# Kernel optimization log

Hardware: AMD Instinct MI355X
Metric: run time of the kernel (lower is better)

Reference implementation:

```python
import jax, jax.numpy as jnp
import numpy as np

N_NODES = 100000
N_EDGES = 1600000
HID = 256
HEADS = 4
HEAD_DIM = HID // HEADS
EPS = 1e-5


def _layernorm(x, g, b):
    mu = jnp.mean(x, axis=-1, keepdims=True)
    var = jnp.mean(jnp.square(x - mu), axis=-1, keepdims=True)
    return (x - mu) * jax.lax.rsqrt(var + EPS) * g + b


def setup_inputs() -> dict:
    key = jax.random.key(0)
    ks = jax.random.split(key, 16)
    s = 0.05  # small init, mimics xavier gain=0.1
    inp = {
        'h': jax.random.normal(ks[0], (N_NODES, HID), jnp.float32),
        'src': jax.random.randint(ks[1], (N_EDGES,), 0, N_NODES, jnp.int32),
        'dst': jax.random.randint(ks[2], (N_EDGES,), 0, N_NODES, jnp.int32),
        'Wq': jax.random.normal(ks[3], (HID, HID), jnp.float32) * s,
        'bq': jnp.zeros((HID,), jnp.float32),
        'Wk': jax.random.normal(ks[4], (HID, HID), jnp.float32) * s,
        'bk': jnp.zeros((HID,), jnp.float32),
        'Wv': jax.random.normal(ks[5], (HID, HID), jnp.float32) * s,
        'bv': jnp.zeros((HID,), jnp.float32),
        'Wo': jax.random.normal(ks[6], (HID, HID), jnp.float32) * s,
        'bo': jnp.zeros((HID,), jnp.float32),
        'W1': jax.random.normal(ks[7], (HID, 2 * HID), jnp.float32) * s,
        'b1': jnp.zeros((2 * HID,), jnp.float32),
        'W2': jax.random.normal(ks[8], (2 * HID, HID), jnp.float32) * s,
        'b2': jnp.zeros((HID,), jnp.float32),
        'g1': jnp.ones((HID,), jnp.float32),
        'be1': jnp.zeros((HID,), jnp.float32),
        'g2': jnp.ones((HID,), jnp.float32),
        'be2': jnp.zeros((HID,), jnp.float32),
    }
    return inp


def reference(h, src, dst, Wq, bq, Wk, bk, Wv, bv, Wo, bo, W1, b1, W2, b2, g1, be1, g2, be2):
    N = h.shape[0]
    scale = HEAD_DIM ** -0.5
    h_norm = _layernorm(h, g1, be1)
    Q = (h_norm @ Wq + bq).reshape(N, HEADS, HEAD_DIM)
    K = (h_norm @ Wk + bk).reshape(N, HEADS, HEAD_DIM)
    V = (h_norm @ Wv + bv).reshape(N, HEADS, HEAD_DIM)

    # per-edge attention logits: q from dst, k from src  -> [E, heads]
    logits = jnp.einsum('ehd,ehd->eh', Q[dst], K[src]) * scale

    # edge softmax grouped by destination node (dgl.ops.edge_softmax)
    seg_max = jax.ops.segment_max(logits, dst, num_segments=N)  # [N, heads]
    e = jnp.exp(logits - seg_max[dst])
    seg_sum = jax.ops.segment_sum(e, dst, num_segments=N)
    w = e / seg_sum[dst]  # [E, heads]

    # message = V[src] * attn ; aggregate by sum over incoming edges
    msg = V[src] * w[:, :, None]  # [E, heads, head_dim]
    h_new = jax.ops.segment_sum(msg, dst, num_segments=N).reshape(N, HID)

    h_attn = h_new @ Wo + bo
    h = h + h_attn  # dropout is identity in eval
    h2 = _layernorm(h, g2, be2)
    ffn = jax.nn.relu(h2 @ W1 + b1) @ W2 + b2
    return h + ffn
```

## Files before the change

### kernel.cpp

```cpp
#include <hip/hip_runtime.h>
#include <hip/hip_bf16.h>

#define NN 100000
#define NE 1600000

typedef __attribute__((ext_vector_type(8))) short bf16x8;
typedef __attribute__((ext_vector_type(4))) float f32x4;
typedef __attribute__((ext_vector_type(2))) float f32x2;
typedef __attribute__((ext_vector_type(2))) unsigned int u32x2;
typedef __attribute__((ext_vector_type(4))) unsigned int u32x4;

__device__ __forceinline__ float bf2f(unsigned short u) {
    union { unsigned int i; float f; } c; c.i = ((unsigned int)u) << 16; return c.f;
}
__device__ __forceinline__ unsigned short f2bf(float f) {
    union { float f; unsigned int i; } c; c.f = f;
    unsigned int lsb = (c.i >> 16) & 1u;
    c.i += 0x7FFFu + lsb;
    return (unsigned short)(c.i >> 16);
}
__device__ __forceinline__ u32x4 pack8bf(f32x4 a, f32x4 b) {
    u32x4 p;
    p.x = f2bf(a[0]) | ((unsigned int)f2bf(a[1]) << 16);
    p.y = f2bf(a[2]) | ((unsigned int)f2bf(a[3]) << 16);
    p.z = f2bf(b[0]) | ((unsigned int)f2bf(b[1]) << 16);
    p.w = f2bf(b[2]) | ((unsigned int)f2bf(b[3]) << 16);
    return p;
}
__device__ __forceinline__ void gload_lds16(const void* g, void* l) {
    __builtin_amdgcn_global_load_lds(
        (const __attribute__((address_space(1))) void*)g,
        (__attribute__((address_space(3))) void*)l, 16, 0, 0);
}

__global__ __launch_bounds__(256) void ln_k(
    const float* __restrict__ x, const float* __restrict__ g,
    const float* __restrict__ b, unsigned short* __restrict__ y, int nrows)
{
    int w = threadIdx.x >> 6, lane = threadIdx.x & 63;
    int row = blockIdx.x * 4 + w;
    if (row >= nrows) return;
    const float4 xv = *(const float4*)(x + (size_t)row * 256 + lane * 4);
    float s  = xv.x + xv.y + xv.z + xv.w;
    float sq = xv.x*xv.x + xv.y*xv.y + xv.z*xv.z + xv.w*xv.w;
    #pragma unroll
    for (int m = 1; m < 64; m <<= 1) {
        s  += __shfl_xor(s,  m);
        sq += __shfl_xor(sq, m);
    }
    float mu  = s * (1.0f / 256.0f);
    float var = sq * (1.0f / 256.0f) - mu * mu;
    float r = rsqrtf(var + 1e-5f);
    float4 gv = *(const float4*)(g + lane * 4);
    float4 bv = *(const float4*)(b + lane * 4);
    ushort4 o;
    o.x = f2bf((xv.x - mu) * r * gv.x + bv.x);
    o.y = f2bf((xv.y - mu) * r * gv.y + bv.y);
    o.z = f2bf((xv.z - mu) * r * gv.z + bv.z);
    o.w = f2bf((xv.w - mu) * r * gv.w + bv.w);
    *(ushort4*)(y + (size_t)row * 256 + lane * 4) = o;
}

__global__ __launch_bounds__(256) void wcv_all_k(
    const float* __restrict__ Wq, const float* __restrict__ Wk, const float* __restrict__ Wv,
    const float* __restrict__ Wo, const float* __restrict__ W1, const float* __restrict__ W2,
    unsigned short* __restrict__ Wqkvt, unsigned short* __restrict__ Wot,
    unsigned short* __restrict__ W1t, unsigned short* __restrict__ W2t,
    const float* __restrict__ bq, const float* __restrict__ bk, const float* __restrict__ bv,
    float* __restrict__ bqkv)
{
    int id = blockIdx.x;
    int t = threadIdx.x;
    if (id == 512) {
        bqkv[t] = bq[t]; bqkv[256 + t] = bk[t]; bqkv[512 + t] = bv[t];
        return;
    }
    const float* W; unsigned short* Wt; int K, N, kx, ny;
    if (id < 192) {
        int grp = id >> 6, l = id & 63;
        W = (grp == 0) ? Wq : ((grp == 1) ? Wk : Wv);
        Wt = Wqkvt + grp * 256 * 256;
        K = 256; N = 256; kx = l & 7; ny = l >> 3;
    } else if (id < 256) {
        int l = id - 192; W = Wo; Wt = Wot; K = 256; N = 256; kx = l & 7; ny = l >> 3;
    } else if (id < 384) {
        int l = id - 256; W = W1; Wt = W1t; K = 256; N = 512; kx = l & 7; ny = l >> 3;
    } else {
        int l = id - 384; W = W2; Wt = W2t; K = 512; N = 256; kx = l & 15; ny = l >> 4;
    }
    __shared__ unsigned short tl[32][33];
    int bk2 = kx * 32, bn = ny * 32;
    int lx = t & 31, ly = t >> 5;
    #pragma unroll
    for (int r = 0; r < 32; r += 8)
        tl[ly + r][lx] = f2bf(W[(size_t)(bk2 + ly + r) * N + bn + lx]);
    __syncthreads();
    #pragma unroll
    for (int r = 0; r < 32; r += 8)
        Wt[(size_t)(bn + ly + r) * K + bk2 + lx] = tl[lx][ly + r];
}

template<int OMODE, bool RELU, bool RES>
__global__ __launch_bounds__(512) void mgemm_k(
    const unsigned short* __restrict__ A, const unsigned short* __restrict__ Wt,
    const float* __restrict__ bias, void* __restrict__ outv, void* __restrict__ out2,
    const void* __restrict__ res, const float* __restrict__ g, const float* __restrict__ be,
    int M, int N, int K)
{
    __shared__ __align__(16) char lds[49152];
    const int t = threadIdx.x;
    const int lane = t & 63;
    const int wid = t >> 6;
    const int wm = wid >> 2, wn = wid & 3;
    const int bm = blockIdx.y * 128, bn = blockIdx.x * 256;

    f32x4 acc[4][4] = {};

    const int ra_s = t >> 2;
    const int sa_s = (t & 3) ^ (ra_s & 3);
    const size_t arow = (size_t)min(bm + ra_s, M - 1) * K + sa_s * 8;
    const int rb0 = t >> 2;
    const int sb0 = (t & 3) ^ (rb0 & 3);
    const int rb1 = (512 + t) >> 2;
    const int sb1 = (t & 3) ^ (rb1 & 3);
    const size_t brow0 = (size_t)(bn + rb0) * K + sb0 * 8;
    const size_t brow1 = (size_t)(bn + rb1) * K + sb1 * 8;

    const int fr = lane & 15, fs = lane >> 4;
    const int rslot = fs ^ (fr & 3);

    const int KS = K >> 5;
    int cur = 0;
    {
        unsigned short* Ab = (unsigned short*)(lds);
        unsigned short* Bb = (unsigned short*)(lds + 16384);
        gload_lds16(A + arow, Ab + t * 8);
        gload_lds16(Wt + brow0, Bb + t * 8);
        gload_lds16(Wt + brow1, Bb + (512 + t) * 8);
    }
    for (int ks = 0; ks < KS; ++ks) {
        __syncthreads();
        if (ks + 1 < KS) {
            int k1 = (ks + 1) << 5;
            unsigned short* Ab = (unsigned short*)(lds + (cur ^ 1) * 8192);
            unsigned short* Bb = (unsigned short*)(lds + 16384 + (cur ^ 1) * 16384);
            gload_lds16(A + arow + k1, Ab + t * 8);
            gload_lds16(Wt + brow0 + k1, Bb + t * 8);
            gload_lds16(Wt + brow1 + k1, Bb + (512 + t) * 8);
        }
        const unsigned short* As = (const unsigned short*)(lds + cur * 8192);
        const unsigned short* Bs = (const unsigned short*)(lds + 16384 + cur * 16384);
        bf16x8 af[4], bf[4];
        #pragma unroll
        for (int fm = 0; fm < 4; ++fm)
            af[fm] = *(const bf16x8*)&As[(wm * 64 + fm * 16 + fr) * 32 + rslot * 8];
        #pragma unroll
        for (int fn = 0; fn < 4; ++fn)
            bf[fn] = *(const bf16x8*)&Bs[(wn * 64 + fn * 16 + fr) * 32 + rslot * 8];
        #pragma unroll
        for (int fm = 0; fm < 4; ++fm)
            #pragma unroll
            for (int fn = 0; fn < 4; ++fn)
                acc[fm][fn] = __builtin_amdgcn_mfma_f32_16x16x32_bf16(
                    af[fm], bf[fn], acc[fm][fn], 0, 0, 0);
        cur ^= 1;
    }
    __syncthreads();

    float* wl = (float*)(lds + wid * 4352);
    float* stats = (float*)(lds + 34816);
    const int rr = lane >> 2;
    const int c4 = (lane & 3) * 16;
    const int qg = lane >> 4;

    #pragma unroll
    for (int fm = 0; fm < 4; ++fm) {
        #pragma unroll
        for (int fn = 0; fn < 4; ++fn)
            #pragma unroll
            for (int i = 0; i < 4; ++i)
                wl[(qg * 4 + i) * 68 + fn * 16 + fr] = acc[fm][fn][i];
        f32x4 v0 = *(const f32x4*)&wl[rr * 68 + c4 + 0];
        f32x4 v1 = *(const f32x4*)&wl[rr * 68 + c4 + 4];
        f32x4 v2 = *(const f32x4*)&wl[rr * 68 + c4 + 8];
        f32x4 v3 = *(const f32x4*)&wl[rr * 68 + c4 + 12];
        const int rowg = bm + wm * 64 + fm * 16 + rr;
        const int colg = bn + wn * 64 + c4;
        if (rowg < M) {
            v0 += *(const f32x4*)&bias[colg + 0];
            v1 += *(const f32x4*)&bias[colg + 4];
            v2 += *(const f32x4*)&bias[colg + 8];
            v3 += *(const f32x4*)&bias[colg + 12];
            if (RES) {
                if (OMODE == 4) {
                    const unsigned short* rp = (const unsigned short*)res + (size_t)rowg * N + colg;
                    u32x4 ra = *(const u32x4*)rp;
                    u32x4 rb = *(const u32x4*)(rp + 8);
                    v0[0] += bf2f(ra.x & 0xffff); v0[1] += bf2f(ra.x >> 16);
                    v0[2] += bf2f(ra.y & 0xffff); v0[3] += bf2f(ra.y >> 16);
                    v1[0] += bf2f(ra.z & 0xffff); v1[1] += bf2f(ra.z >> 16);
                    v1[2] += bf2f(ra.w & 0xffff); v1[3] += bf2f(ra.w >> 16);
                    v2[0] += bf2f(rb.x & 0xffff); v2[1] += bf2f(rb.x >> 16);
                    v2[2] += bf2f(rb.y & 0xffff); v2[3] += bf2f(rb.y >> 16);
                    v3[0] += bf2f(rb.z & 0xffff); v3[1] += bf2f(rb.z >> 16);
                    v3[2] += bf2f(rb.w & 0xffff); v3[3] += bf2f(rb.w >> 16);
                } else {
                    const float* rp = (const float*)res + (size_t)rowg * N + colg;
                    v0 += *(const f32x4*)(rp + 0);
                    v1 += *(const f32x4*)(rp + 4);
                    v2 += *(const f32x4*)(rp + 8);
                    v3 += *(const f32x4*)(rp + 12);
                }
            }
            if (RELU) {
                #pragma unroll
                for (int j = 0; j < 4; ++j) {
                    v0[j] = fmaxf(v0[j], 0.f); v1[j] = fmaxf(v1[j], 0.f);
                    v2[j] = fmaxf(v2[j], 0.f); v3[j] = fmaxf(v3[j], 0.f);
                }
            }
        } else {
            v0 = 0.f; v1 = 0.f; v2 = 0.f; v3 = 0.f;
        }

        if (OMODE == 3) {
            acc[fm][0] = v0; acc[fm][1] = v1; acc[fm][2] = v2; acc[fm][3] = v3;
        } else if (rowg < M) {
            if (OMODE == 0 || OMODE == 4) {
                float* op = (float*)outv + (size_t)rowg * N + colg;
                *(f32x4*)(op + 0) = v0; *(f32x4*)(op + 4) = v1;
                *(f32x4*)(op + 8) = v2; *(f32x4*)(op + 12) = v3;
            } else if (OMODE == 1) {
                unsigned short* op = (unsigned short*)outv + (size_t)rowg * N + colg;
                *(u32x4*)(op + 0) = pack8bf(v0, v1);
                *(u32x4*)(op + 8) = pack8bf(v2, v3);
            } else {
                if (colg < 256) {
                    unsigned short* op = (unsigned short*)outv + (size_t)rowg * 256 + colg;
                    *(u32x4*)(op + 0) = pack8bf(v0, v1);
                    *(u32x4*)(op + 8) = pack8bf(v2, v3);
                } else {
                    u32x4 p8;
                    unsigned int w0, w1, w2, w3;
                    w0 = __builtin_amdgcn_cvt_pk_fp8_f32(v0[0], v0[1], 0, false);
                    w0 = __builtin_amdgcn_cvt_pk_fp8_f32(v0[2], v0[3], w0, true);
                    w1 = __builtin_amdgcn_cvt_pk_fp8_f32(v1[0], v1[1], 0, false);
                    w1 = __builtin_amdgcn_cvt_pk_fp8_f32(v1[2], v1[3], w1, true);
                    w2 = __builtin_amdgcn_cvt_pk_fp8_f32(v2[0], v2[1], 0, false);
                    w2 = __builtin_amdgcn_cvt_pk_fp8_f32(v2[2], v2[3], w2, true);
                    w3 = __builtin_amdgcn_cvt_pk_fp8_f32(v3[0], v3[1], 0, false);
                    w3 = __builtin_amdgcn_cvt_pk_fp8_f32(v3[2], v3[3], w3, true);
                    p8.x = w0; p8.y = w1; p8.z = w2; p8.w = w3;
                    *(u32x4*)((unsigned char*)out2 + (size_t)rowg * 512 + (colg - 256)) = p8;
                }
            }
        }
    }

    if (OMODE == 3) {
        #pragma unroll
        for (int fm = 0; fm < 4; ++fm) {
            float s = 0.f, q = 0.f;
            #pragma unroll
            for (int j = 0; j < 4; ++j)
                #pragma unroll
                for (int c = 0; c < 4; ++c) {
                    float x = acc[fm][j][c];
                    s += x; q += x * x;
                }
            s += __shfl_xor(s, 1); q += __shfl_xor(q, 1);
            s += __shfl_xor(s, 2); q += __shfl_xor(q, 2);
            if ((lane & 3) == 0) {
                int rowl = wm * 64 + fm * 16 + rr;
                stats[rowl * 8 + wn * 2 + 0] = s;
                stats[rowl * 8 + wn * 2 + 1] = q;
            }
        }
        __syncthreads();
        #pragma unroll
        for (int fm = 0; fm < 4; ++fm) {
            const int rowl = wm * 64 + fm * 16 + rr;
            const int rowg = bm + rowl;
            float s = stats[rowl * 8 + 0] + stats[rowl * 8 + 2] + stats[rowl * 8 + 4] + stats[rowl * 8 + 6];
            float q = stats[rowl * 8 + 1] + stats[rowl * 8 + 3] + stats[rowl * 8 + 5] + stats[rowl * 8 + 7];
            float mu = s * (1.0f / 256.0f);
            float var = q * (1.0f / 256.0f) - mu * mu;
            float rstd = rsqrtf(var + 1e-5f);
            const int colg = bn + wn * 64 + c4;
            if (rowg < M) {
                unsigned short* mp = (unsigned short*)out2 + (size_t)rowg * 256 + colg;
                *(u32x4*)(mp + 0) = pack8bf(acc[fm][0], acc[fm][1]);
                *(u32x4*)(mp + 8) = pack8bf(acc[fm][2], acc[fm][3]);
                f32x4 nv[4];
                #pragma unroll
                for (int j = 0; j < 4; ++j) {
                    f32x4 gv = *(const f32x4*)&g[colg + j * 4];
                    f32x4 bv = *(const f32x4*)&be[colg + j * 4];
                    #pragma unroll
                    for (int c = 0; c < 4; ++c)
                        nv[j][c] = (acc[fm][j][c] - mu) * rstd * gv[c] + bv[c];
                }
                unsigned short* op = (unsigned short*)outv + (size_t)rowg * 256 + colg;
                *(u32x4*)(op + 0) = pack8bf(nv[0], nv[1]);
                *(u32x4*)(op + 8) = pack8bf(nv[2], nv[3]);
            }
        }
    }
}

__global__ void degcnt_k(const int* __restrict__ dst, int* __restrict__ deg, int E)
{
    int e = blockIdx.x * blockDim.x + threadIdx.x;
    if (e < E) atomicAdd(deg + dst[e], 1);
}

__global__ __launch_bounds__(1024) void scanA_k(int* __restrict__ a, int* __restrict__ aux, int n)
{
    __shared__ int wsum[16];
    __shared__ int wpre[16];
    int t = threadIdx.x, lane = t & 63, w = t >> 6;
    int i = blockIdx.x * 1024 + t;
    int v = (i < n) ? a[i] : 0;
    int s = v;
    #pragma unroll
    for (int d = 1; d < 64; d <<= 1) {
        int u = __shfl_up(s, d);
        if (lane >= d) s += u;
    }
    if (lane == 63) wsum[w] = s;
    __syncthreads();
    if (t == 0) {
        int run = 0;
        #pragma unroll
        for (int j = 0; j < 16; ++j) { wpre[j] = run; run += wsum[j]; }
        aux[blockIdx.x] = run;
    }
    __syncthreads();
    if (i < n) a[i] = wpre[w] + s - v;
}

__global__ __launch_bounds__(128) void scanB_k(int* __restrict__ aux, int* __restrict__ tot, int nb)
{
    __shared__ int ws[2];
    int t = threadIdx.x, lane = t & 63, w = t >> 6;
    int v = (t < nb) ? aux[t] : 0;
    int s = v;
    #pragma unroll
    for (int d = 1; d < 64; d <<= 1) {
        int u = __shfl_up(s, d);
        if (lane >= d) s += u;
    }
    if (lane == 63) ws[w] = s;
    __syncthreads();
    int add = (w == 1) ? ws[0] : 0;
    if (t < nb) aux[t] = add + s - v;
    if (t == nb - 1) tot[0] = add + s;
}

__global__ __launch_bounds__(1024) void scanC_k(int* __restrict__ a, const int* __restrict__ aux, int n)
{
    int i = blockIdx.x * 1024 + threadIdx.x;
    if (i < n) a[i] += aux[blockIdx.x];
}

__global__ void scatter_k(
    const int* __restrict__ dst, const int* __restrict__ srcarr,
    const int* __restrict__ off, int* __restrict__ cursor,
    int* __restrict__ csr, int E)
{
    int e = blockIdx.x * blockDim.x + threadIdx.x;
    if (e >= E) return;
    int d = dst[e];
    int pos = off[d] + atomicAdd(cursor + d, 1);
    csr[pos] = srcarr[e] << 9;
}

__global__ __launch_bounds__(256) void attn_k(
    const int* __restrict__ csr, const int* __restrict__ off,
    const unsigned short* __restrict__ Q, const unsigned char* __restrict__ KV8,
    unsigned short* __restrict__ hnew)
{
    int w = threadIdx.x >> 6, lane = threadIdx.x & 63;
    int n = blockIdx.x * 4 + w;
    if (n >= NN) return;
    int e0 = off[n], e1 = off[n + 1];

    const unsigned char* KVl = KV8 + lane * 4;

    u32x2 qr = __builtin_nontemporal_load((const u32x2*)(Q + (size_t)n * 256 + lane * 4));
    const float qs = 0.125f * 1.4426950408889634f;
    const float q0 = bf2f((unsigned short)(qr.x & 0xffff)) * qs;
    const float q1 = bf2f((unsigned short)(qr.x >> 16))    * qs;
    const float q2 = bf2f((unsigned short)(qr.y & 0xffff)) * qs;
    const float q3 = bf2f((unsigned short)(qr.y >> 16))    * qs;

    float s = 0.f;
    float a0 = 0.f, a1 = 0.f, a2 = 0.f, a3 = 0.f;

    int i = e0;
    for (; i + 7 < e1; i += 8) {
        int ns[8];
        #pragma unroll
        for (int j = 0; j < 8; ++j) ns[j] = csr[i + j];
        unsigned int kd[8], vd[8];
        #pragma unroll
        for (int j = 0; j < 8; ++j) {
            const unsigned char* r = KVl + (size_t)(unsigned)ns[j];
            kd[j] = *(const unsigned int*)r;
            vd[j] = *(const unsigned int*)(r + 256);
        }
        float l[8];
        #pragma unroll
        for (int j = 0; j < 8; ++j) {
            f32x2 ka = __builtin_amdgcn_cvt_pk_f32_fp8(kd[j], false);
            f32x2 kb = __builtin_amdgcn_cvt_pk_f32_fp8(kd[j], true);
            l[j] = q0 * ka.x + q1 * ka.y + q2 * kb.x + q3 * kb.y;
        }
        #pragma unroll
        for (int m2 = 1; m2 < 16; m2 <<= 1) {
            #pragma unroll
            for (int j = 0; j < 8; ++j) l[j] += __shfl_xor(l[j], m2);
        }
        #pragma unroll
        for (int j = 0; j < 8; ++j) {
            float p = exp2f(l[j]);
            f32x2 va = __builtin_amdgcn_cvt_pk_f32_fp8(vd[j], false);
            f32x2 vb = __builtin_amdgcn_cvt_pk_f32_fp8(vd[j], true);
            s  += p;
            a0 += p * va.x; a1 += p * va.y;
            a2 += p * vb.x; a3 += p * vb.y;
        }
    }
    for (; i + 3 < e1; i += 4) {
        int ns[4];
        #pragma unroll
        for (int j = 0; j < 4; ++j) ns[j] = csr[i + j];
        unsigned int kd[4], vd[4];
        #pragma unroll
        for (int j = 0; j < 4; ++j) {
            const unsigned char* r = KVl + (size_t)(unsigned)ns[j];
            kd[j] = *(const unsigned int*)r;
            vd[j] = *(const unsigned int*)(r + 256);
        }
        float l[4];
        #pragma unroll
        for (int j = 0; j < 4; ++j) {
            f32x2 ka = __builtin_amdgcn_cvt_pk_f32_fp8(kd[j], false);
            f32x2 kb = __builtin_amdgcn_cvt_pk_f32_fp8(kd[j], true);
            l[j] = q0 * ka.x + q1 * ka.y + q2 * kb.x + q3 * kb.y;
        }
        #pragma unroll
        for (int m2 = 1; m2 < 16; m2 <<= 1) {
            #pragma unroll
            for (int j = 0; j < 4; ++j) l[j] += __shfl_xor(l[j], m2);
        }
        #pragma unroll
        for (int j = 0; j < 4; ++j) {
            float p = exp2f(l[j]);
            f32x2 va = __builtin_amdgcn_cvt_pk_f32_fp8(vd[j], false);
            f32x2 vb = __builtin_amdgcn_cvt_pk_f32_fp8(vd[j], true);
            s  += p;
            a0 += p * va.x; a1 += p * va.y;
            a2 += p * vb.x; a3 += p * vb.y;
        }
    }
    for (; i < e1; ++i) {
        const unsigned char* r = KVl + (size_t)(unsigned)csr[i];
        unsigned int kd = *(const unsigned int*)r;
        unsigned int vd = *(const unsigned int*)(r + 256);
        f32x2 ka = __builtin_amdgcn_cvt_pk_f32_fp8(kd, false);
        f32x2 kb = __builtin_amdgcn_cvt_pk_f32_fp8(kd, true);
        float l0 = q0 * ka.x + q1 * ka.y + q2 * kb.x + q3 * kb.y;
        #pragma unroll
        for (int m2 = 1; m2 < 16; m2 <<= 1) l0 += __shfl_xor(l0, m2);
        float p = exp2f(l0);
        f32x2 va = __builtin_amdgcn_cvt_pk_f32_fp8(vd, false);
        f32x2 vb = __builtin_amdgcn_cvt_pk_f32_fp8(vd, true);
        s  += p;
        a0 += p * va.x; a1 += p * va.y;
        a2 += p * vb.x; a3 += p * vb.y;
    }
    float inv = (e1 > e0) ? 1.0f / s : 0.f;
    u32x2 ov;
    ov.x = ((unsigned int)f2bf(a1 * inv) << 16) | f2bf(a0 * inv);
    ov.y = ((unsigned int)f2bf(a3 * inv) << 16) | f2bf(a2 * inv);
    __builtin_nontemporal_store(ov, (u32x2*)(hnew + (size_t)n * 256 + lane * 4));
}

extern "C" void kernel_launch(void* const* d_in, const int* in_sizes, int n_in,
                              void* d_out, int out_size, void* d_ws, size_t ws_size,
                              hipStream_t stream)
{
    if (n_in < 19) return;
    const float* h   = (const float*)d_in[0];
    const int*   src = (const int*)d_in[1];
    const int*   dst = (const int*)d_in[2];
    const float* Wq  = (const float*)d_in[3];
    const float* bq  = (const float*)d_in[4];
    const float* Wk  = (const float*)d_in[5];
    const float* bk  = (const float*)d_in[6];
    const float* Wv  = (const float*)d_in[7];
    const float* bv  = (const float*)d_in[8];
    const float* Wo  = (const float*)d_in[9];
    const float* bo  = (const float*)d_in[10];
    const float* W1  = (const float*)d_in[11];
    const float* b1  = (const float*)d_in[12];
    const float* W2  = (const float*)d_in[13];
    const float* b2  = (const float*)d_in[14];
    const float* g1  = (const float*)d_in[15];
    const float* be1 = (const float*)d_in[16];
    const float* g2  = (const float*)d_in[17];
    const float* be2 = (const float*)d_in[18];
    float* out = (float*)d_out;

    char* w = (char*)d_ws;
    unsigned short* hnormb = (unsigned short*)(w + 0);
    unsigned short* Qb     = (unsigned short*)(w + 51200000);
    unsigned char*  KV8    = (unsigned char*)(w + 102400000);
    int*            degoff = (int*)(w + 153600000);
    int*            cursor = (int*)(w + 154000384);
    int*            csr    = (int*)(w + 154400768);
    unsigned short* Wqkvt  = (unsigned short*)(w + 204800000);
    unsigned short* Wot    = (unsigned short*)(w + 205193216);
    unsigned short* W1t    = (unsigned short*)(w + 205324288);
    unsigned short* W2t    = (unsigned short*)(w + 205586432);
    float*          bqkv   = (float*)(w + 205848576);
    int*            scanaux= (int*)(w + 205851648);
    unsigned short* hnewb  = hnormb;
    unsigned short* h2nb   = hnormb;
    unsigned short* hmidb  = Qb;
    unsigned short* ffnmid = (unsigned short*)(w + 102400000);

    hipMemsetAsync(degoff, 0, 400384, stream);
    hipMemsetAsync(cursor, 0, 400384, stream);

    const int M = NN;
    dim3 blk(256);
    dim3 blk512(512);
    const int SCAN_BLKS = (NN + 1023) / 1024;

    wcv_all_k<<<dim3(513), blk, 0, stream>>>(Wq, Wk, Wv, Wo, W1, W2,
                                             Wqkvt, Wot, W1t, W2t, bq, bk, bv, bqkv);

    degcnt_k<<<dim3((NE + 255) / 256), blk, 0, stream>>>(dst, degoff, NE);
    scanA_k<<<dim3(SCAN_BLKS), dim3(1024), 0, stream>>>(degoff, scanaux, NN);
    scanB_k<<<dim3(1), dim3(128), 0, stream>>>(scanaux, degoff + NN, SCAN_BLKS);
    scanC_k<<<dim3(SCAN_BLKS), dim3(1024), 0, stream>>>(degoff, scanaux, NN);
    scatter_k<<<dim3((NE + 255) / 256), blk, 0, stream>>>(dst, src, degoff, cursor, csr, NE);

    ln_k<<<dim3((NN + 3) / 4), blk, 0, stream>>>(h, g1, be1, hnormb, NN);

    dim3 gq(3, (M + 127) / 128);
    mgemm_k<2, false, false><<<gq, blk512, 0, stream>>>(hnormb, Wqkvt, bqkv, Qb, KV8, nullptr, nullptr, nullptr, M, 768, 256);

    attn_k<<<dim3((NN + 3) / 4), blk, 0, stream>>>(csr, degoff, Qb, KV8, hnewb);

    dim3 go(1, (M + 127) / 128);
    mgemm_k<3, false, true><<<go, blk512, 0, stream>>>(hnewb, Wot, bo, h2nb, hmidb, h, g2, be2, M, 256, 256);

    dim3 g1x(2, (M + 127) / 128);
    mgemm_k<1, true, false><<<g1x, blk512, 0, stream>>>(h2nb, W1t, b1, ffnmid, nullptr, nullptr, nullptr, nullptr, M, 512, 256);
    mgemm_k<4, false, true><<<go, blk512, 0, stream>>>(ffnmid, W2t, b2, out, nullptr, hmidb, nullptr, nullptr, M, 256, 512);
}
```

Before: 599.8 us.

## Split wavefront into four edge groups with 16-lane wide fp8 row loads

Result: no change. 604.4 us (+0.8%).

```diff
diff --git a/kernel.cpp b/kernel.cpp
--- a/kernel.cpp
+++ b/kernel.cpp
@@ -375,6 +375,37 @@
     csr[pos] = srcarr[e] << 9;
 }
 
+__device__ __forceinline__ float dot16_fp8(const float* q, u32x4 kw) {
+    unsigned int wv0 = kw.x, wv1 = kw.y, wv2 = kw.z, wv3 = kw.w;
+    float r = 0.f;
+    f32x2 a, b;
+    a = __builtin_amdgcn_cvt_pk_f32_fp8(wv0, false);
+    b = __builtin_amdgcn_cvt_pk_f32_fp8(wv0, true);
+    r += q[0] * a.x + q[1] * a.y + q[2] * b.x + q[3] * b.y;
+    a = __builtin_amdgcn_cvt_pk_f32_fp8(wv1, false);
+    b = __builtin_amdgcn_cvt_pk_f32_fp8(wv1, true);
+    r += q[4] * a.x + q[5] * a.y + q[6] * b.x + q[7] * b.y;
+    a = __builtin_amdgcn_cvt_pk_f32_fp8(wv2, false);
+    b = __builtin_amdgcn_cvt_pk_f32_fp8(wv2, true);
+    r += q[8] * a.x + q[9] * a.y + q[10] * b.x + q[11] * b.y;
+    a = __builtin_amdgcn_cvt_pk_f32_fp8(wv3, false);
+    b = __builtin_amdgcn_cvt_pk_f32_fp8(wv3, true);
+    r += q[12] * a.x + q[13] * a.y + q[14] * b.x + q[15] * b.y;
+    return r;
+}
+__device__ __forceinline__ void acc16_fp8(float* acc, float p, u32x4 vw) {
+    unsigned int wv[4] = {vw.x, vw.y, vw.z, vw.w};
+    #pragma unroll
+    for (int j = 0; j < 4; ++j) {
+        f32x2 a = __builtin_amdgcn_cvt_pk_f32_fp8(wv[j], false);
+        f32x2 b = __builtin_amdgcn_cvt_pk_f32_fp8(wv[j], true);
+        acc[4 * j + 0] += p * a.x;
+        acc[4 * j + 1] += p * a.y;
+        acc[4 * j + 2] += p * b.x;
+        acc[4 * j + 3] += p * b.y;
+    }
+}
+
 __global__ __launch_bounds__(256) void attn_k(
     const int* __restrict__ csr, const int* __restrict__ off,
     const unsigned short* __restrict__ Q, const unsigned char* __restrict__ KV8,
@@ -384,107 +415,83 @@
     int n = blockIdx.x * 4 + w;
     if (n >= NN) return;
     int e0 = off[n], e1 = off[n + 1];
-
-    const unsigned char* KVl = KV8 + lane * 4;
-
-    u32x2 qr = __builtin_nontemporal_load((const u32x2*)(Q + (size_t)n * 256 + lane * 4));
+    int sl = lane & 15, grp = lane >> 4;
+
     const float qs = 0.125f * 1.4426950408889634f;
-    const float q0 = bf2f((unsigned short)(qr.x & 0xffff)) * qs;
-    const float q1 = bf2f((unsigned short)(qr.x >> 16))    * qs;
-    const float q2 = bf2f((unsigned short)(qr.y & 0xffff)) * qs;
-    const float q3 = bf2f((unsigned short)(qr.y >> 16))    * qs;
-
+    float q[16];
+    {
+        const unsigned short* qp = Q + (size_t)n * 256 + sl * 16;
+        u32x4 qa = *(const u32x4*)qp;
+        u32x4 qb = *(const u32x4*)(qp + 8);
+        unsigned int wq[8] = {qa.x, qa.y, qa.z, qa.w, qb.x, qb.y, qb.z, qb.w};
+        #pragma unroll
+        for (int j = 0; j < 8; ++j) {
+            q[2 * j]     = bf2f((unsigned short)(wq[j] & 0xffff)) * qs;
+            q[2 * j + 1] = bf2f((unsigned short)(wq[j] >> 16)) * qs;
+        }
+    }
+    float acc[16];
+    #pragma unroll
+    for (int d = 0; d < 16; ++d) acc[d] = 0.f;
     float s = 0.f;
-    float a0 = 0.f, a1 = 0.f, a2 = 0.f, a3 = 0.f;
+
+    const unsigned char* KVl = KV8 + sl * 16;
 
     int i = e0;
     for (; i + 7 < e1; i += 8) {
-        int ns[8];
-        #pragma unroll
-        for (int j = 0; j < 8; ++j) ns[j] = csr[i + j];
-        unsigned int kd[8], vd[8];
-        #pragma unroll
-        for (int j = 0; j < 8; ++j) {
-            const unsigned char* r = KVl + (size_t)(unsigned)ns[j];
-            kd[j] = *(const unsigned int*)r;
-            vd[j] = *(const unsigned int*)(r + 256);
-        }
-        float l[8];
-        #pragma unroll
-        for (int j = 0; j < 8; ++j) {
-            f32x2 ka = __builtin_amdgcn_cvt_pk_f32_fp8(kd[j], false);
-            f32x2 kb = __builtin_amdgcn_cvt_pk_f32_fp8(kd[j], true);
-            l[j] = q0 * ka.x + q1 * ka.y + q2 * kb.x + q3 * kb.y;
-        }
-        #pragma unroll
-        for (int m2 = 1; m2 < 16; m2 <<= 1) {
-            #pragma unroll
-            for (int j = 0; j < 8; ++j) l[j] += __shfl_xor(l[j], m2);
-        }
-        #pragma unroll
-        for (int j = 0; j < 8; ++j) {
-            float p = exp2f(l[j]);
-            f32x2 va = __builtin_amdgcn_cvt_pk_f32_fp8(vd[j], false);
-            f32x2 vb = __builtin_amdgcn_cvt_pk_f32_fp8(vd[j], true);
-            s  += p;
-            a0 += p * va.x; a1 += p * va.y;
-            a2 += p * vb.x; a3 += p * vb.y;
-        }
-    }
-    for (; i + 3 < e1; i += 4) {
-        int ns[4];
-        #pragma unroll
-        for (int j = 0; j < 4; ++j) ns[j] = csr[i + j];
-        unsigned int kd[4], vd[4];
-        #pragma unroll
-        for (int j = 0; j < 4; ++j) {
-            const unsigned char* r = KVl + (size_t)(unsigned)ns[j];
-            kd[j] = *(const unsigned int*)r;
-            vd[j] = *(const unsigned int*)(r + 256);
-        }
-        float l[4];
-        #pragma unroll
-        for (int j = 0; j < 4; ++j) {
-            f32x2 ka = __builtin_amdgcn_cvt_pk_f32_fp8(kd[j], false);
-            f32x2 kb = __builtin_amdgcn_cvt_pk_f32_fp8(kd[j], true);
-            l[j] = q0 * ka.x + q1 * ka.y + q2 * kb.x + q3 * kb.y;
-        }
-        #pragma unroll
-        for (int m2 = 1; m2 < 16; m2 <<= 1) {
-            #pragma unroll
-            for (int j = 0; j < 4; ++j) l[j] += __shfl_xor(l[j], m2);
-        }
-        #pragma unroll
-        for (int j = 0; j < 4; ++j) {
-            float p = exp2f(l[j]);
-            f32x2 va = __builtin_amdgcn_cvt_pk_f32_fp8(vd[j], false);
-            f32x2 vb = __builtin_amdgcn_cvt_pk_f32_fp8(vd[j], true);
-            s  += p;
-            a0 += p * va.x; a1 += p * va.y;
-            a2 += p * vb.x; a3 += p * vb.y;
-        }
-    }
-    for (; i < e1; ++i) {
-        const unsigned char* r = KVl + (size_t)(unsigned)csr[i];
-        unsigned int kd = *(const unsigned int*)r;
-        unsigned int vd = *(const unsigned int*)(r + 256);
-        f32x2 ka = __builtin_amdgcn_cvt_pk_f32_fp8(kd, false);
-        f32x2 kb = __builtin_amdgcn_cvt_pk_f32_fp8(kd, true);
-        float l0 = q0 * ka.x + q1 * ka.y + q2 * kb.x + q3 * kb.y;
-        #pragma unroll
-        for (int m2 = 1; m2 < 16; m2 <<= 1) l0 += __shfl_xor(l0, m2);
-        float p = exp2f(l0);
-        f32x2 va = __builtin_amdgcn_cvt_pk_f32_fp8(vd, false);
-        f32x2 vb = __builtin_amdgcn_cvt_pk_f32_fp8(vd, true);
-        s  += p;
-        a0 += p * va.x; a1 += p * va.y;
-        a2 += p * vb.x; a3 += p * vb.y;
-    }
+        int o0 = csr[i + grp];
+        int o1 = csr[i + 4 + grp];
+        u32x4 k0 = *(const u32x4*)(KVl + (unsigned)o0);
+        u32x4 k1 = *(const u32x4*)(KVl + (unsigned)o1);
+        u32x4 v0 = *(const u32x4*)(KVl + (unsigned)o0 + 256);
+        u32x4 v1 = *(const u32x4*)(KVl + (unsigned)o1 + 256);
+        float l0 = dot16_fp8(q, k0);
+        float l1 = dot16_fp8(q, k1);
+        l0 += __shfl_xor(l0, 1); l1 += __shfl_xor(l1, 1);
+        l0 += __shfl_xor(l0, 2); l1 += __shfl_xor(l1, 2);
+        float p0 = exp2f(l0);
+        float p1 = exp2f(l1);
+        s += p0 + p1;
+        acc16_fp8(acc, p0, v0);
+        acc16_fp8(acc, p1, v1);
+    }
+    for (; i < e1; i += 4) {
+        int rem = e1 - i;
+        int idx = i + grp;
+        int o0 = csr[(idx < e1) ? idx : (e1 - 1)];
+        u32x4 k0 = *(const u32x4*)(KVl + (unsigned)o0);
+        u32x4 v0 = *(const u32x4*)(KVl + (unsigned)o0 + 256);
+        float l0 = dot16_fp8(q, k0);
+        l0 += __shfl_xor(l0, 1);
+        l0 += __shfl_xor(l0, 2);
+        float p0 = (grp < rem) ? exp2f(l0) : 0.f;
+        s += p0;
+        acc16_fp8(acc, p0, v0);
+    }
+
+    #pragma unroll
+    for (int d = 0; d < 16; ++d) {
+        acc[d] += __shfl_xor(acc[d], 16);
+        acc[d] += __shfl_xor(acc[d], 32);
+    }
+    s += __shfl_xor(s, 16);
+    s += __shfl_xor(s, 32);
+
     float inv = (e1 > e0) ? 1.0f / s : 0.f;
-    u32x2 ov;
-    ov.x = ((unsigned int)f2bf(a1 * inv) << 16) | f2bf(a0 * inv);
-    ov.y = ((unsigned int)f2bf(a3 * inv) << 16) | f2bf(a2 * inv);
-    __builtin_nontemporal_store(ov, (u32x2*)(hnew + (size_t)n * 256 + lane * 4));
+    if (grp == 0) {
+        u32x4 oa, ob;
+        oa.x = f2bf(acc[0] * inv)  | ((unsigned int)f2bf(acc[1] * inv) << 16);
+        oa.y = f2bf(acc[2] * inv)  | ((unsigned int)f2bf(acc[3] * inv) << 16);
+        oa.z = f2bf(acc[4] * inv)  | ((unsigned int)f2bf(acc[5] * inv) << 16);
+        oa.w = f2bf(acc[6] * inv)  | ((unsigned int)f2bf(acc[7] * inv) << 16);
+        ob.x = f2bf(acc[8] * inv)  | ((unsigned int)f2bf(acc[9] * inv) << 16);
+        ob.y = f2bf(acc[10] * inv) | ((unsigned int)f2bf(acc[11] * inv) << 16);
+        ob.z = f2bf(acc[12] * inv) | ((unsigned int)f2bf(acc[13] * inv) << 16);
+        ob.w = f2bf(acc[14] * inv) | ((unsigned int)f2bf(acc[15] * inv) << 16);
+        unsigned short* op = hnew + (size_t)n * 256 + sl * 16;
+        __builtin_nontemporal_store(oa, (u32x4*)op);
+        __builtin_nontemporal_store(ob, (u32x4*)(op + 8));
+    }
 }
 
 extern "C" void kernel_launch(void* const* d_in, const int* in_sizes, int n_in,
```

## Remap GEMM workgroups per XCD and simplify attention gather indexing

Applied to the files above, without the earlier changes.

Measured after the change: 594.2 us. About the same (-0.9%).

```diff
diff --git a/kernel.cpp b/kernel.cpp
--- a/kernel.cpp
+++ b/kernel.cpp
@@ -26,6 +26,10 @@
     p.z = f2bf(b[0]) | ((unsigned int)f2bf(b[1]) << 16);
     p.w = f2bf(b[2]) | ((unsigned int)f2bf(b[3]) << 16);
     return p;
+}
+__device__ __forceinline__ unsigned int pack4fp8(f32x4 v) {
+    unsigned int w = __builtin_amdgcn_cvt_pk_fp8_f32(v[0], v[1], 0, false);
+    return __builtin_amdgcn_cvt_pk_fp8_f32(v[2], v[3], w, true);
 }
 __device__ __forceinline__ void gload_lds16(const void* g, void* l) {
     __builtin_amdgcn_global_load_lds(
@@ -100,7 +104,7 @@
         Wt[(size_t)(bn + ly + r) * K + bk2 + lx] = tl[lx][ly + r];
 }
 
-template<int OMODE, bool RELU, bool RES>
+template<int NBX, int OMODE, bool RELU, bool RES>
 __global__ __launch_bounds__(512) void mgemm_k(
     const unsigned short* __restrict__ A, const unsigned short* __restrict__ Wt,
     const float* __restrict__ bias, void* __restrict__ outv, void* __restrict__ out2,
@@ -112,7 +116,19 @@
     const int lane = t & 63;
     const int wid = t >> 6;
     const int wm = wid >> 2, wn = wid & 3;
-    const int bm = blockIdx.y * 128, bn = blockIdx.x * 256;
+
+    int bmi, bni;
+    if (NBX > 0) {
+        const int nwg = gridDim.x;
+        const int q = nwg >> 3, r = nwg & 7;
+        const int xcd = blockIdx.x & 7, idx = blockIdx.x >> 3;
+        const int wgid = (xcd < r) ? (xcd * (q + 1) + idx)
+                                   : (r * (q + 1) + (xcd - r) * q + idx);
+        bmi = wgid / NBX; bni = wgid - bmi * NBX;
+    } else {
+        bmi = blockIdx.y; bni = blockIdx.x;
+    }
+    const int bm = bmi * 128, bn = bni * 256;
 
     f32x4 acc[4][4] = {};
 
@@ -241,16 +257,8 @@
                     *(u32x4*)(op + 8) = pack8bf(v2, v3);
                 } else {
                     u32x4 p8;
-                    unsigned int w0, w1, w2, w3;
-                    w0 = __builtin_amdgcn_cvt_pk_fp8_f32(v0[0], v0[1], 0, false);
-                    w0 = __builtin_amdgcn_cvt_pk_fp8_f32(v0[2], v0[3], w0, true);
-                    w1 = __builtin_amdgcn_cvt_pk_fp8_f32(v1[0], v1[1], 0, false);
-                    w1 = __builtin_amdgcn_cvt_pk_fp8_f32(v1[2], v1[3], w1, true);
-                    w2 = __builtin_amdgcn_cvt_pk_fp8_f32(v2[0], v2[1], 0, false);
-                    w2 = __builtin_amdgcn_cvt_pk_fp8_f32(v2[2], v2[3], w2, true);
-                    w3 = __builtin_amdgcn_cvt_pk_fp8_f32(v3[0], v3[1], 0, false);
-                    w3 = __builtin_amdgcn_cvt_pk_fp8_f32(v3[2], v3[3], w3, true);
-                    p8.x = w0; p8.y = w1; p8.z = w2; p8.w = w3;
+                    p8.x = pack4fp8(v0); p8.y = pack4fp8(v1);
+                    p8.z = pack4fp8(v2); p8.w = pack4fp8(v3);
                     *(u32x4*)((unsigned char*)out2 + (size_t)rowg * 512 + (colg - 256)) = p8;
                 }
             }
@@ -372,7 +380,7 @@
     if (e >= E) return;
     int d = dst[e];
     int pos = off[d] + atomicAdd(cursor + d, 1);
-    csr[pos] = srcarr[e] << 9;
+    csr[pos] = srcarr[e];
 }
 
 __global__ __launch_bounds__(256) void attn_k(
@@ -385,14 +393,11 @@
     if (n >= NN) return;
     int e0 = off[n], e1 = off[n + 1];
 
-    const unsigned char* KVl = KV8 + lane * 4;
-
     u32x2 qr = __builtin_nontemporal_load((const u32x2*)(Q + (size_t)n * 256 + lane * 4));
-    const float qs = 0.125f * 1.4426950408889634f;
-    const float q0 = bf2f((unsigned short)(qr.x & 0xffff)) * qs;
-    const float q1 = bf2f((unsigned short)(qr.x >> 16))    * qs;
-    const float q2 = bf2f((unsigned short)(qr.y & 0xffff)) * qs;
-    const float q3 = bf2f((unsigned short)(qr.y >> 16))    * qs;
+    const float q0 = bf2f((unsigned short)(qr.x & 0xffff)) * 0.125f;
+    const float q1 = bf2f((unsigned short)(qr.x >> 16))    * 0.125f;
+    const float q2 = bf2f((unsigned short)(qr.y & 0xffff)) * 0.125f;
+    const float q3 = bf2f((unsigned short)(qr.y >> 16))    * 0.125f;
 
     float s = 0.f;
     float a0 = 0.f, a1 = 0.f, a2 = 0.f, a3 = 0.f;
@@ -405,7 +410,7 @@
         unsigned int kd[8], vd[8];
         #pragma unroll
         for (int j = 0; j < 8; ++j) {
-            const unsigned char* r = KVl + (size_t)(unsigned)ns[j];
+            const unsigned char* r = KV8 + (size_t)ns[j] * 512 + lane * 4;
             kd[j] = *(const unsigned int*)r;
             vd[j] = *(const unsigned int*)(r + 256);
         }
@@ -423,7 +428,7 @@
         }
         #pragma unroll
         for (int j = 0; j < 8; ++j) {
-            float p = exp2f(l[j]);
+            float p = __expf(l[j]);
             f32x2 va = __builtin_amdgcn_cvt_pk_f32_fp8(vd[j], false);
             f32x2 vb = __builtin_amdgcn_cvt_pk_f32_fp8(vd[j], true);
             s  += p;
@@ -438,7 +443,7 @@
         unsigned int kd[4], vd[4];
         #pragma unroll
         for (int j = 0; j < 4; ++j) {
-            const unsigned char* r = KVl + (size_t)(unsigned)ns[j];
+            const unsigned char* r = KV8 + (size_t)ns[j] * 512 + lane * 4;
             kd[j] = *(const unsigned int*)r;
             vd[j] = *(const unsigned int*)(r + 256);
         }
@@ -456,7 +461,7 @@
         }
         #pragma unroll
         for (int j = 0; j < 4; ++j) {
-            float p = exp2f(l[j]);
+            float p = __expf(l[j]);
             f32x2 va = __builtin_amdgcn_cvt_pk_f32_fp8(vd[j], false);
             f32x2 vb = __builtin_amdgcn_cvt_pk_f32_fp8(vd[j], true);
             s  += p;
@@ -465,7 +470,8 @@
         }
     }
     for (; i < e1; ++i) {
-        const unsigned char* r = KVl + (size_t)(unsigned)csr[i];
+        int n0 = csr[i];
+        const unsigned char* r = KV8 + (size_t)n0 * 512 + lane * 4;
         unsigned int kd = *(const unsigned int*)r;
         unsigned int vd = *(const unsigned int*)(r + 256);
         f32x2 ka = __builtin_amdgcn_cvt_pk_f32_fp8(kd, false);
@@ -473,7 +479,7 @@
         float l0 = q0 * ka.x + q1 * ka.y + q2 * kb.x + q3 * kb.y;
         #pragma unroll
         for (int m2 = 1; m2 < 16; m2 <<= 1) l0 += __shfl_xor(l0, m2);
-        float p = exp2f(l0);
+        float p = __expf(l0);
         f32x2 va = __builtin_amdgcn_cvt_pk_f32_fp8(vd, false);
         f32x2 vb = __builtin_amdgcn_cvt_pk_f32_fp8(vd, true);
         s  += p;
@@ -537,6 +543,7 @@
     const int M = NN;
     dim3 blk(256);
     dim3 blk512(512);
+    const int MB = (M + 127) / 128;
     const int SCAN_BLKS = (NN + 1023) / 1024;
 
     wcv_all_k<<<dim3(513), blk, 0, stream>>>(Wq, Wk, Wv, Wo, W1, W2,
@@ -550,15 +557,17 @@
 
     ln_k<<<dim3((NN + 3) / 4), blk, 0, stream>>>(h, g1, be1, hnormb, NN);
 
-    dim3 gq(3, (M + 127) / 128);
-    mgemm_k<2, false, false><<<gq, blk512, 0, stream>>>(hnormb, Wqkvt, bqkv, Qb, KV8, nullptr, nullptr, nullptr, M, 768, 256);
+    mgemm_k<3, 2, false, false><<<dim3(3 * MB), blk512, 0, stream>>>(
+        hnormb, Wqkvt, bqkv, Qb, KV8, nullptr, nullptr, nullptr, M, 768, 256);
 
     attn_k<<<dim3((NN + 3) / 4), blk, 0, stream>>>(csr, degoff, Qb, KV8, hnewb);
 
-    dim3 go(1, (M + 127) / 128);
-    mgemm_k<3, false, true><<<go, blk512, 0, stream>>>(hnewb, Wot, bo, h2nb, hmidb, h, g2, be2, M, 256, 256);
-
-    dim3 g1x(2, (M + 127) / 128);
-    mgemm_k<1, true, false><<<g1x, blk512, 0, stream>>>(h2nb, W1t, b1, ffnmid, nullptr, nullptr, nullptr, nullptr, M, 512, 256);
-    mgemm_k<4, false, true><<<go, blk512, 0, stream>>>(ffnmid, W2t, b2, out, nullptr, hmidb, nullptr, nullptr, M, 256, 512);
-}
+    dim3 go(1, MB);
+    mgemm_k<0, 3, false, true><<<go, blk512, 0, stream>>>(
+        hnewb, Wot, bo, h2nb, hmidb, h, g2, be2, M, 256, 256);
+
+    mgemm_k<2, 1, true, false><<<dim3(2 * MB), blk512, 0, stream>>>(
+        h2nb, W1t, b1, ffnmid, nullptr, nullptr, nullptr, nullptr, M, 512, 256);
+    mgemm_k<0, 4, false, true><<<go, blk512, 0, stream>>>(
+        ffnmid, W2t, b2, out, nullptr, hmidb, nullptr, nullptr, M, 256, 512);
+}
```
